# Kernel optimization log

Hardware: AMD Instinct MI355X
Metric: run time of the kernel (lower is better)

The kernel has to match this reference:

```python
import jax, jax.numpy as jnp
import numpy as np

DIM = 1024
SCALE = 1.0 / np.sqrt(DIM).astype(np.float32)


def setup_inputs() -> dict:
    key = jax.random.key(0)
    ks = jax.random.split(key, 8)
    B, S, D = 4, 2048, DIM
    x = jax.random.normal(ks[0], (B, S, D), dtype=jnp.float32)
    mask = jnp.zeros((S, S), dtype=jnp.float32)  # additive mask, broadcast over batch
    # learned params (nn.Linear: y = x @ W.T + b); store W already transposed for x @ W
    init = 1.0 / np.sqrt(D)
    Wq = jax.random.uniform(ks[1], (D, D), jnp.float32, -init, init)
    bq = jax.random.uniform(ks[2], (D,), jnp.float32, -init, init)
    Wk = jax.random.uniform(ks[3], (D, D), jnp.float32, -init, init)
    bk = jax.random.uniform(ks[4], (D,), jnp.float32, -init, init)
    Wv = jax.random.uniform(ks[5], (D, D), jnp.float32, -init, init)
    bv = jax.random.uniform(ks[6], (D,), jnp.float32, -init, init)
    return {"x": x, "mask": mask, "Wq": Wq, "bq": bq, "Wk": Wk, "bk": bk, "Wv": Wv, "bv": bv}


def reference(x, mask, Wq, bq, Wk, bk, Wv, bv):
    # single-head full-dim attention, scaled by 1/sqrt(dim) (as in the source)
    q = x @ Wq + bq                      # [B, S, D]
    k = x @ Wk + bk                      # [B, S, D]
    v = x @ Wv + bv                      # [B, S, D]
    scores = jnp.einsum('bqd,bkd->bqk', q, k) * SCALE  # [B, S, S]
    scores = scores + mask               # additive mask, broadcast
    attn = jax.nn.softmax(scores, axis=-1)
    # dropout(p=0.1) is identity in eval mode
    return jnp.einsum('bqk,bkd->bqd', attn, v)  # [B, S, D]
```

## Files before the change

kernel.cpp:

```cpp
#include <hip/hip_runtime.h>

typedef unsigned short u16;
typedef unsigned int u32;

typedef __attribute__((ext_vector_type(8))) short bf16x8;
typedef __attribute__((ext_vector_type(4))) float f32x4;

static __device__ __forceinline__ u16 f2bf(float f) {
    u32 u = __float_as_uint(f);
    u32 r = (u + 0x7FFFu + ((u >> 16) & 1u)) >> 16;
    return (u16)r;
}
static __device__ __forceinline__ float bf2f(u16 h) {
    return __uint_as_float(((u32)h) << 16);
}
static __device__ __forceinline__ u32 pack2(float a, float b) {
    return (u32)f2bf(a) | ((u32)f2bf(b) << 16);
}

__global__ __launch_bounds__(256) void convert_bf16_kernel(const float* __restrict__ x,
                                                           u16* __restrict__ y, int n4) {
    int i = blockIdx.x * 256 + threadIdx.x;
    if (i < n4) {
        float4 v = ((const float4*)x)[i];
        ushort4 o;
        o.x = f2bf(v.x); o.y = f2bf(v.y); o.z = f2bf(v.z); o.w = f2bf(v.w);
        ((ushort4*)y)[i] = o;
    }
}

__global__ __launch_bounds__(256) void transpose3_to_bf16_kernel(
    const float* __restrict__ W0, const float* __restrict__ W1, const float* __restrict__ W2,
    u16* __restrict__ T0, u16* __restrict__ T1, u16* __restrict__ T2, int D) {
    __shared__ float t[32][33];
    const float* W = (blockIdx.z == 0) ? W0 : (blockIdx.z == 1) ? W1 : W2;
    u16* WT = (blockIdx.z == 0) ? T0 : (blockIdx.z == 1) ? T1 : T2;
    int bx = blockIdx.x, by = blockIdx.y;
    int tx = threadIdx.x, ty = threadIdx.y;
#pragma unroll
    for (int i = ty; i < 32; i += 8)
        t[i][tx] = W[(long)(by * 32 + i) * D + bx * 32 + tx];
    __syncthreads();
#pragma unroll
    for (int i = ty; i < 32; i += 8)
        WT[(long)(bx * 32 + i) * D + by * 32 + tx] = f2bf(t[tx][i]);
}

__global__ __launch_bounds__(256) void concat_bias_kernel(const float* __restrict__ a,
                                                          const float* __restrict__ b,
                                                          float* __restrict__ o, int n) {
    int i = blockIdx.x * 256 + threadIdx.x;
    if (i < 2 * n) o[i] = (i < n) ? a[i] : b[i - n];
}

__global__ __launch_bounds__(256, 4) void gemm_bt_kernel(
    const u16* __restrict__ A, int lda, long sA,
    const u16* __restrict__ B, int ldb, long sB,
    void* __restrict__ C, int ldc, long sC, int c_bf16,
    const float* __restrict__ bias, int bias_mode,
    const float* __restrict__ madd, int mask_ld,
    float* __restrict__ rowsum, int rs_mode, int rs_ld, int swapxy,
    float scale, int K) {
    __shared__ __align__(16) u16 SMEM[2][256 * 32];
    const int bz = blockIdx.z;
    const u16* Ab = A + (long)bz * sA;
    const u16* Bb = B + (long)bz * sB;
    const int bxi = swapxy ? blockIdx.y : blockIdx.x;
    const int byi = swapxy ? blockIdx.x : blockIdx.y;
    const int tm = byi * 128, tn = bxi * 128;
    const int tid = threadIdx.x, wave = tid >> 6, lane = tid & 63;
    const int wm = (wave >> 1) * 64, wn = (wave & 1) * 64;
    const int lr = lane >> 2, c = lane & 3;
    const int fm = lane & 15, fq = lane >> 4;

    f32x4 acc[4][4];
#pragma unroll
    for (int i = 0; i < 4; i++)
#pragma unroll
        for (int j = 0; j < 4; j++) acc[i][j] = (f32x4){0.f, 0.f, 0.f, 0.f};

    const int T = K >> 5;

    auto stage = [&](int t, int buf) {
        u16* As = &SMEM[buf][0];
        u16* Bs = &SMEM[buf][128 * 32];
#pragma unroll
        for (int r = 0; r < 2; r++) {
            const int rl = r * 64 + wave * 16;
            const int row = rl + lr;
            const int kc = (t << 5) + ((c ^ ((row ^ (row >> 2)) & 3)) << 3);
            const u16* ga = Ab + (long)(tm + row) * lda + kc;
            const u16* gb = Bb + (long)(tn + row) * ldb + kc;
            __builtin_amdgcn_global_load_lds((const __attribute__((address_space(1))) void*)ga,
                                             (__attribute__((address_space(3))) void*)&As[rl * 32],
                                             16, 0, 0);
            __builtin_amdgcn_global_load_lds((const __attribute__((address_space(1))) void*)gb,
                                             (__attribute__((address_space(3))) void*)&Bs[rl * 32],
                                             16, 0, 0);
        }
    };

    stage(0, 0);
    __syncthreads();
    for (int t = 0; t < T; t++) {
        const int cur = t & 1;
        if (t + 1 < T) stage(t + 1, cur ^ 1);
        const u16* As = &SMEM[cur][0];
        const u16* Bs = &SMEM[cur][128 * 32];
        bf16x8 af[4], bfr[4];
#pragma unroll
        for (int i = 0; i < 4; i++) {
            int row = wm + i * 16 + fm;
            af[i] = *(const bf16x8*)&As[row * 32 + ((fq ^ ((row ^ (row >> 2)) & 3)) << 3)];
        }
#pragma unroll
        for (int j = 0; j < 4; j++) {
            int row = wn + j * 16 + fm;
            bfr[j] = *(const bf16x8*)&Bs[row * 32 + ((fq ^ ((row ^ (row >> 2)) & 3)) << 3)];
        }
#pragma unroll
        for (int i = 0; i < 4; i++)
#pragma unroll
            for (int j = 0; j < 4; j++)
                acc[i][j] = __builtin_amdgcn_mfma_f32_16x16x32_bf16(af[i], bfr[j], acc[i][j], 0, 0, 0);
        if (t + 1 < T) __syncthreads();
    }
    __syncthreads();

    float* EP = (float*)&SMEM[0][0] + wave * 1088;
    const int row16 = lane >> 2, cb = (lane & 3) * 16;
    float4 bc[4];
    if (bias_mode == 1) {
#pragma unroll
        for (int q = 0; q < 4; q++) bc[q] = *(const float4*)&bias[tn + wn + cb + q * 4];
    }
#pragma unroll
    for (int i = 0; i < 4; i++) {
#pragma unroll
        for (int j = 0; j < 4; j++)
#pragma unroll
            for (int r = 0; r < 4; r++)
                EP[(fq * 4 + r) * 68 + j * 16 + fm] = acc[i][j][r];
        const long grow = tm + wm + i * 16 + row16;
        float rb = (bias_mode == 2) ? bias[grow] : 0.f;
        float4 t4[4];
#pragma unroll
        for (int q = 0; q < 4; q++) {
            float4 v = *(const float4*)&EP[row16 * 68 + cb + q * 4];
            v.x = v.x * scale + rb; v.y = v.y * scale + rb;
            v.z = v.z * scale + rb; v.w = v.w * scale + rb;
            if (bias_mode == 1) { v.x += bc[q].x; v.y += bc[q].y; v.z += bc[q].z; v.w += bc[q].w; }
            if (madd) {
                float4 m4 = *(const float4*)&madd[grow * mask_ld + tn + wn + cb + q * 4];
                v.x += m4.x; v.y += m4.y; v.z += m4.z; v.w += m4.w;
            }
            t4[q] = v;
        }
        if (rs_mode == 1) {
            float s = 0.f;
#pragma unroll
            for (int q = 0; q < 4; q++) {
                t4[q].x = __expf(t4[q].x); t4[q].y = __expf(t4[q].y);
                t4[q].z = __expf(t4[q].z); t4[q].w = __expf(t4[q].w);
                s += t4[q].x + t4[q].y + t4[q].z + t4[q].w;
            }
            s += __shfl_xor(s, 1);
            s += __shfl_xor(s, 2);
            if ((lane & 3) == 0) atomicAdd(&rowsum[(long)bz * rs_ld + grow], s);
        } else if (rs_mode == 2) {
            float inv = 1.f / rowsum[(long)bz * rs_ld + grow];
#pragma unroll
            for (int q = 0; q < 4; q++) {
                t4[q].x *= inv; t4[q].y *= inv; t4[q].z *= inv; t4[q].w *= inv;
            }
        }
        if (c_bf16) {
            u16* dst = (u16*)C + (long)bz * sC + grow * ldc + tn + wn + cb;
            uint4 o0 = {pack2(t4[0].x, t4[0].y), pack2(t4[0].z, t4[0].w),
                        pack2(t4[1].x, t4[1].y), pack2(t4[1].z, t4[1].w)};
            uint4 o1 = {pack2(t4[2].x, t4[2].y), pack2(t4[2].z, t4[2].w),
                        pack2(t4[3].x, t4[3].y), pack2(t4[3].z, t4[3].w)};
            *(uint4*)dst = o0;
            *(uint4*)(dst + 8) = o1;
        } else {
            float* dst = (float*)C + (long)bz * sC + grow * ldc + tn + wn + cb;
#pragma unroll
            for (int q = 0; q < 4; q++) *(float4*)(dst + q * 4) = t4[q];
        }
    }
}

extern "C" void kernel_launch(void* const* d_in, const int* in_sizes, int n_in,
                              void* d_out, int out_size, void* d_ws, size_t ws_size,
                              hipStream_t stream) {
    const float* x    = (const float*)d_in[0];
    const float* mask = (const float*)d_in[1];
    const float* Wq   = (const float*)d_in[2];
    const float* bq   = (const float*)d_in[3];
    const float* Wk   = (const float*)d_in[4];
    const float* bk   = (const float*)d_in[5];
    const float* Wv   = (const float*)d_in[6];
    const float* bv   = (const float*)d_in[7];
    float* out = (float*)d_out;

    const int B = 4, S = 2048, D = 1024;
    const long MS = (long)B * S;

    size_t need = (size_t)MS * D * 2 + (size_t)(2 * D) * D * 2 + (size_t)D * D * 2
                + (size_t)(2 * D) * 4 + (size_t)MS * (2 * D) * 2 + (size_t)D * MS * 2
                + (size_t)B * S * S * 2 + (size_t)B * S * 4;
    if (ws_size < need) return;

    char* ws = (char*)d_ws;
    u16*  xb   = (u16*)ws;  ws += (long)MS * D * 2;
    u16*  wqkt = (u16*)ws;  ws += (long)(2 * D) * D * 2;
    u16*  wvt  = (u16*)ws;  ws += (long)D * D * 2;
    float* bqk = (float*)ws; ws += (long)(2 * D) * 4;
    u16*  QK   = (u16*)ws;  ws += (long)MS * (2 * D) * 2;
    u16*  VT   = (u16*)ws;  ws += (long)D * MS * 2;
    u16*  sc   = (u16*)ws;  ws += (long)B * S * S * 2;
    float* rsum = (float*)ws; ws += (long)B * S * 4;

    const float SCALE = 0.03125f;

    hipMemsetAsync(rsum, 0, (size_t)B * S * 4, stream);

    convert_bf16_kernel<<<(int)((MS * D / 4 + 255) / 256), 256, 0, stream>>>(x, xb, (int)(MS * D / 4));
    transpose3_to_bf16_kernel<<<dim3(32, 32, 3), dim3(32, 8), 0, stream>>>(
        Wq, Wk, Wv, wqkt, wqkt + (long)D * D, wvt, D);
    concat_bias_kernel<<<8, 256, 0, stream>>>(bq, bk, bqk, D);

    gemm_bt_kernel<<<dim3(2 * D / 128, (int)(MS / 128), 1), 256, 0, stream>>>(
        xb, D, 0, wqkt, D, 0, QK, 2 * D, 0, 1, bqk, 1, nullptr, 0,
        nullptr, 0, 0, 0, 1.0f, D);
    gemm_bt_kernel<<<dim3((int)(MS / 128), D / 128, 1), 256, 0, stream>>>(
        wvt, D, 0, xb, D, 0, VT, (int)MS, 0, 1, bv, 2, nullptr, 0,
        nullptr, 0, 0, 0, 1.0f, D);

    gemm_bt_kernel<<<dim3(S / 128, S / 128, B), 256, 0, stream>>>(
        QK, 2 * D, (long)S * 2 * D, QK + D, 2 * D, (long)S * 2 * D, sc, S, (long)S * S, 1,
        nullptr, 0, mask, S, rsum, 1, S, 0, SCALE, D);

    gemm_bt_kernel<<<dim3(S / 128, D / 128, B), 256, 0, stream>>>(
        sc, S, (long)S * S, VT, (int)MS, (long)S, out, D, (long)S * D, 0,
        nullptr, 0, nullptr, 0, rsum, 2, S, 1, 1.0f, S);
}
```

Before: 311.7 us.

## Fuse prep kernels, merge QKV GEMMs, convert mask to bf16, XCD-aware block mapping

Merges the input conversion, weight transpose, bias concat and rowsum zeroing into one prep kernel, and converts the mask to bf16 there. The Q/K and V^T projection GEMMs now run in a single launch. The score and PV GEMMs remap block indices so that tiles of the same batch land on the same XCD, which should improve L2 reuse. Together these cut launch count and mask read bandwidth, but the mask is now rounded to bf16 and one extra S×S conversion pass is added to prep.

```diff
diff --git a/kernel.cpp b/kernel.cpp
--- a/kernel.cpp
+++ b/kernel.cpp
@@ -18,56 +18,67 @@
     return (u32)f2bf(a) | ((u32)f2bf(b) << 16);
 }
 
-__global__ __launch_bounds__(256) void convert_bf16_kernel(const float* __restrict__ x,
-                                                           u16* __restrict__ y, int n4) {
-    int i = blockIdx.x * 256 + threadIdx.x;
-    if (i < n4) {
+__global__ __launch_bounds__(256) void prep_kernel(
+    const float* __restrict__ x, u16* __restrict__ xb,
+    const float* __restrict__ mask, u16* __restrict__ maskb,
+    const float* __restrict__ Wq, const float* __restrict__ Wk, const float* __restrict__ Wv,
+    u16* __restrict__ T0, u16* __restrict__ T1, u16* __restrict__ T2,
+    const float* __restrict__ bq, const float* __restrict__ bk,
+    float* __restrict__ bqk, float* __restrict__ rsum) {
+    const int D = 1024;
+    int bid = blockIdx.x;
+    const int tid = threadIdx.x;
+    if (bid < 8192) {
+        long i = (long)bid * 256 + tid;
         float4 v = ((const float4*)x)[i];
-        ushort4 o;
-        o.x = f2bf(v.x); o.y = f2bf(v.y); o.z = f2bf(v.z); o.w = f2bf(v.w);
-        ((ushort4*)y)[i] = o;
-    }
-}
-
-__global__ __launch_bounds__(256) void transpose3_to_bf16_kernel(
-    const float* __restrict__ W0, const float* __restrict__ W1, const float* __restrict__ W2,
-    u16* __restrict__ T0, u16* __restrict__ T1, u16* __restrict__ T2, int D) {
-    __shared__ float t[32][33];
-    const float* W = (blockIdx.z == 0) ? W0 : (blockIdx.z == 1) ? W1 : W2;
-    u16* WT = (blockIdx.z == 0) ? T0 : (blockIdx.z == 1) ? T1 : T2;
-    int bx = blockIdx.x, by = blockIdx.y;
-    int tx = threadIdx.x, ty = threadIdx.y;
-#pragma unroll
-    for (int i = ty; i < 32; i += 8)
-        t[i][tx] = W[(long)(by * 32 + i) * D + bx * 32 + tx];
-    __syncthreads();
-#pragma unroll
-    for (int i = ty; i < 32; i += 8)
-        WT[(long)(bx * 32 + i) * D + by * 32 + tx] = f2bf(t[tx][i]);
-}
-
-__global__ __launch_bounds__(256) void concat_bias_kernel(const float* __restrict__ a,
-                                                          const float* __restrict__ b,
-                                                          float* __restrict__ o, int n) {
-    int i = blockIdx.x * 256 + threadIdx.x;
-    if (i < 2 * n) o[i] = (i < n) ? a[i] : b[i - n];
-}
-
-__global__ __launch_bounds__(256, 4) void gemm_bt_kernel(
-    const u16* __restrict__ A, int lda, long sA,
-    const u16* __restrict__ B, int ldb, long sB,
-    void* __restrict__ C, int ldc, long sC, int c_bf16,
+        ushort4 o; o.x = f2bf(v.x); o.y = f2bf(v.y); o.z = f2bf(v.z); o.w = f2bf(v.w);
+        ((ushort4*)xb)[i] = o;
+        return;
+    }
+    bid -= 8192;
+    if (bid < 4096) {
+        long i = (long)bid * 256 + tid;
+        float4 v = ((const float4*)mask)[i];
+        ushort4 o; o.x = f2bf(v.x); o.y = f2bf(v.y); o.z = f2bf(v.z); o.w = f2bf(v.w);
+        ((ushort4*)maskb)[i] = o;
+        return;
+    }
+    bid -= 4096;
+    if (bid < 3072) {
+        __shared__ float t[32][33];
+        const int z = bid >> 10, loc = bid & 1023;
+        const int bx = loc & 31, by = loc >> 5;
+        const float* W = (z == 0) ? Wq : (z == 1) ? Wk : Wv;
+        u16* WT = (z == 0) ? T0 : (z == 1) ? T1 : T2;
+        const int tx = tid & 31, ty = tid >> 5;
+#pragma unroll
+        for (int i = ty; i < 32; i += 8)
+            t[i][tx] = W[(long)(by * 32 + i) * D + bx * 32 + tx];
+        __syncthreads();
+#pragma unroll
+        for (int i = ty; i < 32; i += 8)
+            WT[(long)(bx * 32 + i) * D + by * 32 + tx] = f2bf(t[tx][i]);
+        return;
+    }
+    bid -= 3072;
+    if (bid < 8) {
+        int i = bid * 256 + tid;
+        bqk[i] = (i < 1024) ? bq[i] : bk[i - 1024];
+        return;
+    }
+    bid -= 8;
+    rsum[bid * 256 + tid] = 0.f;
+}
+
+static __device__ __forceinline__ void gemm_core(
+    u16* __restrict__ SM,
+    const u16* __restrict__ Ab, int lda,
+    const u16* __restrict__ Bb, int ldb,
+    void* __restrict__ Cb, int ldc, int c_bf16,
     const float* __restrict__ bias, int bias_mode,
-    const float* __restrict__ madd, int mask_ld,
-    float* __restrict__ rowsum, int rs_mode, int rs_ld, int swapxy,
-    float scale, int K) {
-    __shared__ __align__(16) u16 SMEM[2][256 * 32];
-    const int bz = blockIdx.z;
-    const u16* Ab = A + (long)bz * sA;
-    const u16* Bb = B + (long)bz * sB;
-    const int bxi = swapxy ? blockIdx.y : blockIdx.x;
-    const int byi = swapxy ? blockIdx.x : blockIdx.y;
-    const int tm = byi * 128, tn = bxi * 128;
+    const u16* __restrict__ madd, int mask_ld,
+    float* __restrict__ rowsum, int rs_mode,
+    float scale, int K, int tm, int tn) {
     const int tid = threadIdx.x, wave = tid >> 6, lane = tid & 63;
     const int wm = (wave >> 1) * 64, wn = (wave & 1) * 64;
     const int lr = lane >> 2, c = lane & 3;
@@ -82,8 +93,8 @@
     const int T = K >> 5;
 
     auto stage = [&](int t, int buf) {
-        u16* As = &SMEM[buf][0];
-        u16* Bs = &SMEM[buf][128 * 32];
+        u16* As = SM + buf * 8192;
+        u16* Bs = As + 4096;
 #pragma unroll
         for (int r = 0; r < 2; r++) {
             const int rl = r * 64 + wave * 16;
@@ -105,8 +116,8 @@
     for (int t = 0; t < T; t++) {
         const int cur = t & 1;
         if (t + 1 < T) stage(t + 1, cur ^ 1);
-        const u16* As = &SMEM[cur][0];
-        const u16* Bs = &SMEM[cur][128 * 32];
+        const u16* As = SM + cur * 8192;
+        const u16* Bs = As + 4096;
         bf16x8 af[4], bfr[4];
 #pragma unroll
         for (int i = 0; i < 4; i++) {
@@ -127,7 +138,7 @@
     }
     __syncthreads();
 
-    float* EP = (float*)&SMEM[0][0] + wave * 1088;
+    float* EP = (float*)SM + wave * 1088;
     const int row16 = lane >> 2, cb = (lane & 3) * 16;
     float4 bc[4];
     if (bias_mode == 1) {
@@ -151,8 +162,8 @@
             v.z = v.z * scale + rb; v.w = v.w * scale + rb;
             if (bias_mode == 1) { v.x += bc[q].x; v.y += bc[q].y; v.z += bc[q].z; v.w += bc[q].w; }
             if (madd) {
-                float4 m4 = *(const float4*)&madd[grow * mask_ld + tn + wn + cb + q * 4];
-                v.x += m4.x; v.y += m4.y; v.z += m4.z; v.w += m4.w;
+                ushort4 m4 = *(const ushort4*)&madd[grow * mask_ld + tn + wn + cb + q * 4];
+                v.x += bf2f(m4.x); v.y += bf2f(m4.y); v.z += bf2f(m4.z); v.w += bf2f(m4.w);
             }
             t4[q] = v;
         }
@@ -166,16 +177,16 @@
             }
             s += __shfl_xor(s, 1);
             s += __shfl_xor(s, 2);
-            if ((lane & 3) == 0) atomicAdd(&rowsum[(long)bz * rs_ld + grow], s);
+            if ((lane & 3) == 0) atomicAdd(&rowsum[grow], s);
         } else if (rs_mode == 2) {
-            float inv = 1.f / rowsum[(long)bz * rs_ld + grow];
+            float inv = 1.f / rowsum[grow];
 #pragma unroll
             for (int q = 0; q < 4; q++) {
                 t4[q].x *= inv; t4[q].y *= inv; t4[q].z *= inv; t4[q].w *= inv;
             }
         }
         if (c_bf16) {
-            u16* dst = (u16*)C + (long)bz * sC + grow * ldc + tn + wn + cb;
+            u16* dst = (u16*)Cb + grow * ldc + tn + wn + cb;
             uint4 o0 = {pack2(t4[0].x, t4[0].y), pack2(t4[0].z, t4[0].w),
                         pack2(t4[1].x, t4[1].y), pack2(t4[1].z, t4[1].w)};
             uint4 o1 = {pack2(t4[2].x, t4[2].y), pack2(t4[2].z, t4[2].w),
@@ -183,11 +194,63 @@
             *(uint4*)dst = o0;
             *(uint4*)(dst + 8) = o1;
         } else {
-            float* dst = (float*)C + (long)bz * sC + grow * ldc + tn + wn + cb;
+            float* dst = (float*)Cb + grow * ldc + tn + wn + cb;
 #pragma unroll
             for (int q = 0; q < 4; q++) *(float4*)(dst + q * 4) = t4[q];
         }
     }
+}
+
+__global__ __launch_bounds__(256, 4) void gemm_qkvt_kernel(
+    const u16* __restrict__ xb, const u16* __restrict__ wqkt, const u16* __restrict__ wvt,
+    u16* __restrict__ QK, u16* __restrict__ VT,
+    const float* __restrict__ bqk, const float* __restrict__ bv) {
+    __shared__ __align__(16) u16 SM[2][256 * 32];
+    const int D = 1024, MS = 8192;
+    const int id = blockIdx.x;
+    if (id < 1024) {
+        gemm_core(&SM[0][0], xb, D, wqkt, D, QK, 2 * D, 1, bqk, 1, nullptr, 0,
+                  nullptr, 0, 1.0f, D, (id >> 4) * 128, (id & 15) * 128);
+    } else {
+        const int f = id - 1024;
+        gemm_core(&SM[0][0], wvt, D, xb, D, VT, MS, 1, bv, 2, nullptr, 0,
+                  nullptr, 0, 1.0f, D, (f >> 6) * 128, (f & 63) * 128);
+    }
+}
+
+__global__ __launch_bounds__(256, 4) void gemm_sc_kernel(
+    const u16* __restrict__ QK, u16* __restrict__ sc,
+    const u16* __restrict__ maskb, float* __restrict__ rsum, float scale) {
+    __shared__ __align__(16) u16 SM[2][256 * 32];
+    const int S = 2048, D = 1024;
+    const int lin = blockIdx.x;
+    const int xcd = lin & 7, r = lin >> 3;
+    const int bx = r & 15, ylo = (r >> 4) & 7;
+    const int bz = xcd >> 1, by = (xcd & 1) * 8 + ylo;
+    gemm_core(&SM[0][0],
+              QK + (long)bz * S * 2 * D, 2 * D,
+              QK + D + (long)bz * S * 2 * D, 2 * D,
+              sc + (long)bz * S * S, S, 1, nullptr, 0,
+              maskb, S, rsum + (long)bz * S, 1,
+              scale, D, by * 128, bx * 128);
+}
+
+__global__ __launch_bounds__(256, 4) void gemm_pv_kernel(
+    const u16* __restrict__ sc, const u16* __restrict__ VT,
+    float* __restrict__ out, const float* __restrict__ rsum) {
+    __shared__ __align__(16) u16 SM[2][256 * 32];
+    const int S = 2048, D = 1024, MS = 8192;
+    const int xcd = blockIdx.x;
+    const int s = blockIdx.y + 16 * blockIdx.z;
+    const int bz = xcd >> 1;
+    const int byi = (xcd & 1) * 8 + (s >> 3);
+    const int bxi = s & 7;
+    gemm_core(&SM[0][0],
+              sc + (long)bz * S * S, S,
+              VT + (long)bz * S, MS,
+              out + (long)bz * S * D, D, 0, nullptr, 0,
+              nullptr, 0, (float*)(rsum + (long)bz * S), 2,
+              1.0f, S, byi * 128, bxi * 128);
 }
 
 extern "C" void kernel_launch(void* const* d_in, const int* in_sizes, int n_in,
@@ -208,7 +271,7 @@
 
     size_t need = (size_t)MS * D * 2 + (size_t)(2 * D) * D * 2 + (size_t)D * D * 2
                 + (size_t)(2 * D) * 4 + (size_t)MS * (2 * D) * 2 + (size_t)D * MS * 2
-                + (size_t)B * S * S * 2 + (size_t)B * S * 4;
+                + (size_t)B * S * S * 2 + (size_t)B * S * 4 + (size_t)S * S * 2;
     if (ws_size < need) return;
 
     char* ws = (char*)d_ws;
@@ -220,28 +283,14 @@
     u16*  VT   = (u16*)ws;  ws += (long)D * MS * 2;
     u16*  sc   = (u16*)ws;  ws += (long)B * S * S * 2;
     float* rsum = (float*)ws; ws += (long)B * S * 4;
+    u16*  maskb = (u16*)ws; ws += (long)S * S * 2;
 
     const float SCALE = 0.03125f;
 
-    hipMemsetAsync(rsum, 0, (size_t)B * S * 4, stream);
-
-    convert_bf16_kernel<<<(int)((MS * D / 4 + 255) / 256), 256, 0, stream>>>(x, xb, (int)(MS * D / 4));
-    transpose3_to_bf16_kernel<<<dim3(32, 32, 3), dim3(32, 8), 0, stream>>>(
-        Wq, Wk, Wv, wqkt, wqkt + (long)D * D, wvt, D);
-    concat_bias_kernel<<<8, 256, 0, stream>>>(bq, bk, bqk, D);
-
-    gemm_bt_kernel<<<dim3(2 * D / 128, (int)(MS / 128), 1), 256, 0, stream>>>(
-        xb, D, 0, wqkt, D, 0, QK, 2 * D, 0, 1, bqk, 1, nullptr, 0,
-        nullptr, 0, 0, 0, 1.0f, D);
-    gemm_bt_kernel<<<dim3((int)(MS / 128), D / 128, 1), 256, 0, stream>>>(
-        wvt, D, 0, xb, D, 0, VT, (int)MS, 0, 1, bv, 2, nullptr, 0,
-        nullptr, 0, 0, 0, 1.0f, D);
-
-    gemm_bt_kernel<<<dim3(S / 128, S / 128, B), 256, 0, stream>>>(
-        QK, 2 * D, (long)S * 2 * D, QK + D, 2 * D, (long)S * 2 * D, sc, S, (long)S * S, 1,
-        nullptr, 0, mask, S, rsum, 1, S, 0, SCALE, D);
-
-    gemm_bt_kernel<<<dim3(S / 128, D / 128, B), 256, 0, stream>>>(
-        sc, S, (long)S * S, VT, (int)MS, (long)S, out, D, (long)S * D, 0,
-        nullptr, 0, nullptr, 0, rsum, 2, S, 1, 1.0f, S);
-}
+    prep_kernel<<<15400, 256, 0, stream>>>(x, xb, mask, maskb, Wq, Wk, Wv,
+                                           wqkt, wqkt + (long)D * D, wvt,
+                                           bq, bk, bqk, rsum);
+    gemm_qkvt_kernel<<<1536, 256, 0, stream>>>(xb, wqkt, wvt, QK, VT, bqk, bv);
+    gemm_sc_kernel<<<1024, 256, 0, stream>>>(QK, sc, maskb, rsum, SCALE);
+    gemm_pv_kernel<<<dim3(8, 16, 4), 256, 0, stream>>>(sc, VT, out, rsum);
+}
```

Measured after the change: 277.5 us. 1.12x faster.
